# Optimization experiments

Hardware: AMD Instinct MI355X
Metric: run time of the kernel (lower is better)

Reference implementation:

```python
import jax, jax.numpy as jnp
import numpy as np

SIZE = 7  # spatial size, matches init kwarg


def setup_inputs() -> dict:
    key = jax.random.key(0)
    k1, k2 = jax.random.split(key, 2)
    N, C, H, W = 256, 2048, SIZE, SIZE
    x = jax.random.normal(k1, (N, C, H, W), dtype=jnp.float32)
    # nn.Linear(2*C, 2): weight (2, 2C), bias (2,)
    Wlin = jax.random.normal(k2, (2, 2 * C), dtype=jnp.float32) * 0.02
    b = jnp.zeros((2,), dtype=jnp.float32)
    return {"x": x, "Wlin": Wlin, "b": b}


def reference(x, Wlin, b):
    N, C, H, W = x.shape
    HW = H * W
    size = SIZE
    # (N, HW, C) token view
    rx = x.reshape(N, C, HW).transpose(0, 2, 1)
    # index of max mean-activation token per sample
    idx = jnp.argmax(jnp.mean(rx, axis=-1), axis=-1)  # (N,)
    bidx = jnp.arange(N)
    max_feat = rx[bidx, idx]  # (N, C)
    # concat(max_feat, rx) @ Wlin.T + b, split to avoid materializing (N,HW,2C)
    W1, W2 = Wlin[:, :C], Wlin[:, C:]
    pred = jax.nn.relu(
        jnp.einsum('npc,oc->npo', rx, W2) + (max_feat @ W1.T)[:, None, :] + b
    )  # (N, HW, 2)
    # zero out prediction at the anchor token
    pred = pred.at[bidx, idx].set(0.0)
    # basic label grid (i, j)
    ii, jj = jnp.meshgrid(jnp.arange(H), jnp.arange(W), indexing='ij')
    label = jnp.stack([ii, jj], axis=-1).reshape(HW, 2).astype(x.dtype)  # (HW, 2)
    anchor = label[idx][:, None, :]  # (N, 1, 2)
    rel = (label[None, :, :] - anchor) / size  # (N, HW, 2)
    rel_dist = jnp.sqrt(jnp.sum(rel ** 2, axis=-1))  # (N, HW)
    rel_angle = (jnp.arctan2(rel[..., 1], rel[..., 0]) / jnp.pi + 1) / 2  # (N, HW)
    dist_loss = (pred[..., 0] - rel_dist) ** 2
    gap = pred[..., 1] - rel_angle
    gap = jnp.where(gap < 0, gap + 1, gap)
    gap = gap - jnp.mean(gap, axis=-1, keepdims=True)
    return (dist_loss + gap ** 2).reshape(N, H, W)
```

## Files before the change

### kernel.cpp

```cpp
#include <hip/hip_runtime.h>
#include <hip/hip_bf16.h>
#include <math.h>

#define N_BATCH 256
#define C_CH    2048
#define HW      49
#define SIZE7   7
#define S_SPLIT 8
#define C_PER   (C_CH / S_SPLIT)
#define BLOCK   256
#define WAVES   4

__global__ __launch_bounds__(BLOCK) void rpp_partial_kernel(
    const float* __restrict__ x, const float* __restrict__ Wlin,
    float* __restrict__ ws) {
  const int bid  = blockIdx.x;
  const int n    = bid >> 3;
  const int s    = bid & (S_SPLIT - 1);
  const int tid  = threadIdx.x;
  const int lane = tid & 63;
  const int wave = tid >> 6;

  __shared__ __align__(16) float w_s[4][C_PER];
  __shared__ float red[WAVES][5][64];

  const int cbase = s * C_PER;
  for (int i = tid; i < 4 * C_PER; i += BLOCK) {
    const int q = i >> 8;
    const int c = i & (C_PER - 1);
    const int off = (q & 1) * (2 * C_CH) + (q >> 1) * C_CH;
    w_s[q][c] = Wlin[off + cbase + c];
  }
  __syncthreads();

  const int lp = (lane < HW) ? lane : 0;
  const int wbase = wave * 64;
  const float* xp = x + (size_t)n * C_CH * HW + (size_t)(cbase + wbase) * HW + lp;

  float a0 = 0.f, a1 = 0.f, a2 = 0.f, a3 = 0.f, a4 = 0.f;
#pragma unroll 4
  for (int c = 0; c < 64; c += 4, xp += 4 * HW) {
    const float v0 = xp[0 * HW];
    const float v1 = xp[1 * HW];
    const float v2 = xp[2 * HW];
    const float v3 = xp[3 * HW];
    const float4 w0 = *(const float4*)&w_s[0][wbase + c];
    const float4 w1 = *(const float4*)&w_s[1][wbase + c];
    const float4 w2 = *(const float4*)&w_s[2][wbase + c];
    const float4 w3 = *(const float4*)&w_s[3][wbase + c];
    a0 += (v0 + v1) + (v2 + v3);
    a1 = fmaf(v0, w0.x, fmaf(v1, w0.y, fmaf(v2, w0.z, fmaf(v3, w0.w, a1))));
    a2 = fmaf(v0, w1.x, fmaf(v1, w1.y, fmaf(v2, w1.z, fmaf(v3, w1.w, a2))));
    a3 = fmaf(v0, w2.x, fmaf(v1, w2.y, fmaf(v2, w2.z, fmaf(v3, w2.w, a3))));
    a4 = fmaf(v0, w3.x, fmaf(v1, w3.y, fmaf(v2, w3.z, fmaf(v3, w3.w, a4))));
  }

  red[wave][0][lane] = a0;
  red[wave][1][lane] = a1;
  red[wave][2][lane] = a2;
  red[wave][3][lane] = a3;
  red[wave][4][lane] = a4;
  __syncthreads();

  for (int i = tid; i < 5 * 64; i += BLOCK) {
    const int q = i >> 6;
    const int l = i & 63;
    ws[(size_t)bid * 320 + i] =
        red[0][q][l] + red[1][q][l] + red[2][q][l] + red[3][q][l];
  }
}

__global__ __launch_bounds__(64) void rpp_final_kernel(
    const float* __restrict__ ws, const float* __restrict__ b,
    float* __restrict__ out) {
  const int n = blockIdx.x;
  const int lane = threadIdx.x;

  float s0 = 0.f, s1 = 0.f, s2 = 0.f, s3 = 0.f, s4 = 0.f;
  const float* base = ws + (size_t)n * S_SPLIT * 320;
#pragma unroll
  for (int s = 0; s < S_SPLIT; s++) {
    const float* bs = base + s * 320;
    s0 += bs[0 * 64 + lane];
    s1 += bs[1 * 64 + lane];
    s2 += bs[2 * 64 + lane];
    s3 += bs[3 * 64 + lane];
    s4 += bs[4 * 64 + lane];
  }

  float v = (lane < HW) ? s0 : -INFINITY;
  int vi = lane;
#pragma unroll
  for (int off = 32; off; off >>= 1) {
    const float ov = __shfl_down(v, off);
    const int oi = __shfl_down(vi, off);
    if (ov > v || (ov == v && oi < vi)) { v = ov; vi = oi; }
  }
  const int idx = __shfl(vi, 0);

  const float anc0 = __shfl(s1, idx);
  const float anc1 = __shfl(s2, idx);
  const float b0 = b[0], b1 = b[1];

  float pred0 = fmaxf(s3 + anc0 + b0, 0.f);
  float pred1 = fmaxf(s4 + anc1 + b1, 0.f);
  if (lane == idx) { pred0 = 0.f; pred1 = 0.f; }

  const int li = lane / SIZE7, lj = lane % SIZE7;
  const int ai = idx / SIZE7, aj = idx % SIZE7;
  const float ri = (float)(li - ai) * (1.0f / SIZE7);
  const float rj = (float)(lj - aj) * (1.0f / SIZE7);
  const float rdist = sqrtf(ri * ri + rj * rj);
  const float rangle = atan2f(rj, ri) * 0.15915494309189535f + 0.5f;

  float dl = pred0 - rdist;
  dl *= dl;
  float gap = pred1 - rangle;
  if (gap < 0.f) gap += 1.f;

  float g = (lane < HW) ? gap : 0.f;
#pragma unroll
  for (int off = 32; off; off >>= 1) g += __shfl_down(g, off);
  const float mean = __shfl(g, 0) * (1.0f / HW);
  gap -= mean;

  if (lane < HW) out[(size_t)n * HW + lane] = dl + gap * gap;
}

extern "C" void kernel_launch(void* const* d_in, const int* in_sizes, int n_in,
                              void* d_out, int out_size, void* d_ws, size_t ws_size,
                              hipStream_t stream) {
  const float* x    = (const float*)d_in[0];
  const float* Wlin = (const float*)d_in[1];
  const float* b    = (const float*)d_in[2];
  float* out = (float*)d_out;
  float* ws  = (float*)d_ws;

  hipLaunchKernelGGL(rpp_partial_kernel, dim3(N_BATCH * S_SPLIT), dim3(BLOCK), 0,
                     stream, x, Wlin, ws);
  hipLaunchKernelGGL(rpp_final_kernel, dim3(N_BATCH), dim3(64), 0,
                     stream, ws, b, out);
}
```

Before: 154.8 us.

## Fuse partial and final kernels into one block-per-sample kernel

Replaces the two-kernel split (8 channel-split blocks per sample writing to a workspace, then a finalize kernel) with one 1024-thread block per sample that reduces across 16 waves in shared memory and computes the output directly. This removes the second launch and the workspace round trip. In exchange the grid shrinks to 256 large blocks, which lowers parallelism and occupancy for a memory-bound read of about 100 MB, and every block copies the full 32 KB weight matrix into shared memory.

New measurement: 155.8 us. About the same (+0.7%).

```diff
diff --git a/kernel.cpp b/kernel.cpp
--- a/kernel.cpp
+++ b/kernel.cpp
@@ -6,48 +6,49 @@
 #define C_CH    2048
 #define HW      49
 #define SIZE7   7
-#define S_SPLIT 8
-#define C_PER   (C_CH / S_SPLIT)
-#define BLOCK   256
-#define WAVES   4
+#define BLOCK   1024
+#define WAVES   16
+#define C_PER_W (C_CH / WAVES)
 
-__global__ __launch_bounds__(BLOCK) void rpp_partial_kernel(
+__global__ __launch_bounds__(BLOCK) void rpp_fused_kernel(
     const float* __restrict__ x, const float* __restrict__ Wlin,
-    float* __restrict__ ws) {
-  const int bid  = blockIdx.x;
-  const int n    = bid >> 3;
-  const int s    = bid & (S_SPLIT - 1);
+    const float* __restrict__ b, float* __restrict__ out) {
+  const int n    = blockIdx.x;
   const int tid  = threadIdx.x;
   const int lane = tid & 63;
   const int wave = tid >> 6;
 
-  __shared__ __align__(16) float w_s[4][C_PER];
+  __shared__ __align__(16) float wlin_s[2 * 2 * C_CH];
   __shared__ float red[WAVES][5][64];
 
-  const int cbase = s * C_PER;
-  for (int i = tid; i < 4 * C_PER; i += BLOCK) {
-    const int q = i >> 8;
-    const int c = i & (C_PER - 1);
-    const int off = (q & 1) * (2 * C_CH) + (q >> 1) * C_CH;
-    w_s[q][c] = Wlin[off + cbase + c];
+  {
+    const float4* src = (const float4*)Wlin;
+    float4* dst = (float4*)wlin_s;
+#pragma unroll
+    for (int i = tid; i < 2 * C_CH; i += BLOCK) dst[i] = src[i];
   }
   __syncthreads();
 
+  const float* w1r0 = wlin_s;
+  const float* w1r1 = wlin_s + 4096;
+  const float* w2r0 = wlin_s + 2048;
+  const float* w2r1 = wlin_s + 6144;
+
   const int lp = (lane < HW) ? lane : 0;
-  const int wbase = wave * 64;
-  const float* xp = x + (size_t)n * C_CH * HW + (size_t)(cbase + wbase) * HW + lp;
+  const int cbase = wave * C_PER_W;
+  const float* xp = x + (size_t)n * C_CH * HW + (size_t)cbase * HW + lp;
 
   float a0 = 0.f, a1 = 0.f, a2 = 0.f, a3 = 0.f, a4 = 0.f;
 #pragma unroll 4
-  for (int c = 0; c < 64; c += 4, xp += 4 * HW) {
+  for (int c = 0; c < C_PER_W; c += 4, xp += 4 * HW) {
     const float v0 = xp[0 * HW];
     const float v1 = xp[1 * HW];
     const float v2 = xp[2 * HW];
     const float v3 = xp[3 * HW];
-    const float4 w0 = *(const float4*)&w_s[0][wbase + c];
-    const float4 w1 = *(const float4*)&w_s[1][wbase + c];
-    const float4 w2 = *(const float4*)&w_s[2][wbase + c];
-    const float4 w3 = *(const float4*)&w_s[3][wbase + c];
+    const float4 w0 = *(const float4*)&w1r0[cbase + c];
+    const float4 w1 = *(const float4*)&w1r1[cbase + c];
+    const float4 w2 = *(const float4*)&w2r0[cbase + c];
+    const float4 w3 = *(const float4*)&w2r1[cbase + c];
     a0 += (v0 + v1) + (v2 + v3);
     a1 = fmaf(v0, w0.x, fmaf(v1, w0.y, fmaf(v2, w0.z, fmaf(v3, w0.w, a1))));
     a2 = fmaf(v0, w1.x, fmaf(v1, w1.y, fmaf(v2, w1.z, fmaf(v3, w1.w, a2))));
@@ -62,30 +63,16 @@
   red[wave][4][lane] = a4;
   __syncthreads();
 
-  for (int i = tid; i < 5 * 64; i += BLOCK) {
-    const int q = i >> 6;
-    const int l = i & 63;
-    ws[(size_t)bid * 320 + i] =
-        red[0][q][l] + red[1][q][l] + red[2][q][l] + red[3][q][l];
-  }
-}
-
-__global__ __launch_bounds__(64) void rpp_final_kernel(
-    const float* __restrict__ ws, const float* __restrict__ b,
-    float* __restrict__ out) {
-  const int n = blockIdx.x;
-  const int lane = threadIdx.x;
+  if (wave != 0) return;
 
   float s0 = 0.f, s1 = 0.f, s2 = 0.f, s3 = 0.f, s4 = 0.f;
-  const float* base = ws + (size_t)n * S_SPLIT * 320;
 #pragma unroll
-  for (int s = 0; s < S_SPLIT; s++) {
-    const float* bs = base + s * 320;
-    s0 += bs[0 * 64 + lane];
-    s1 += bs[1 * 64 + lane];
-    s2 += bs[2 * 64 + lane];
-    s3 += bs[3 * 64 + lane];
-    s4 += bs[4 * 64 + lane];
+  for (int w = 0; w < WAVES; w++) {
+    s0 += red[w][0][lane];
+    s1 += red[w][1][lane];
+    s2 += red[w][2][lane];
+    s3 += red[w][3][lane];
+    s4 += red[w][4][lane];
   }
 
   float v = (lane < HW) ? s0 : -INFINITY;
@@ -134,10 +121,8 @@
   const float* Wlin = (const float*)d_in[1];
   const float* b    = (const float*)d_in[2];
   float* out = (float*)d_out;
-  float* ws  = (float*)d_ws;
+  (void)d_ws; (void)ws_size;
 
-  hipLaunchKernelGGL(rpp_partial_kernel, dim3(N_BATCH * S_SPLIT), dim3(BLOCK), 0,
-                     stream, x, Wlin, ws);
-  hipLaunchKernelGGL(rpp_final_kernel, dim3(N_BATCH), dim3(64), 0,
-                     stream, ws, b, out);
+  hipLaunchKernelGGL(rpp_fused_kernel, dim3(N_BATCH), dim3(BLOCK), 0,
+                     stream, x, Wlin, b, out);
 }
```
